# Kernel optimization log

Measured on AMD Instinct MI355X. Metric: run time of the kernel, lower is better.

## Reference

```python
import jax, jax.numpy as jnp
import numpy as np

THR = 0.01        # config['thr']
BORDER_RM = 2     # config['border_rm']
TEMP = 0.1        # config['dsmax_temperature']


def setup_inputs() -> dict:
    key = jax.random.key(0)
    k0, k1 = jax.random.split(key)
    N, C = 2, 256
    h0c, w0c, h1c, w1c = 60, 80, 60, 80
    feat_c0 = jax.random.normal(k0, (N, h0c * w0c, C), dtype=jnp.float32)
    feat_c1 = jax.random.normal(k1, (N, h1c * w1c, C), dtype=jnp.float32)
    return {"feat_c0": feat_c0, "feat_c1": feat_c1,
            "h0c": h0c, "w0c": w0c, "h1c": h1c, "w1c": w1c}


def _mask_border(m, b):
    # m: [N, H0, W0, H1, W1] bool; zero out a border of width b on all 4 grid axes
    m = m.at[:, :b].set(False)
    m = m.at[:, :, :b].set(False)
    m = m.at[:, :, :, :b].set(False)
    m = m.at[:, :, :, :, :b].set(False)
    m = m.at[:, -b:].set(False)
    m = m.at[:, :, -b:].set(False)
    m = m.at[:, :, :, -b:].set(False)
    m = m.at[:, :, :, :, -b:].set(False)
    return m


def reference(feat_c0, feat_c1, h0c, w0c, h1c, w1c):
    N, L, C = feat_c0.shape
    S = feat_c1.shape[1]
    # feats are each scaled by C**-0.5, then similarity divided by temperature
    sim = jnp.einsum('nlc,nsc->nls', feat_c0, feat_c1) / (C * TEMP)
    # dual softmax
    conf = jax.nn.softmax(sim, axis=1) * jax.nn.softmax(sim, axis=2)  # [N,L,S]

    # threshold + border removal
    mask = conf > THR
    mask = _mask_border(mask.reshape(N, h0c, w0c, h1c, w1c), BORDER_RM)
    mask = mask.reshape(N, L, S)

    # mutual nearest neighbour
    mask = mask & (conf == conf.max(axis=2, keepdims=True)) \
                & (conf == conf.max(axis=1, keepdims=True))

    # dense, fixed-shape match extraction (torch version uses torch.where)
    mask_v = mask.any(axis=2)                       # [N,L] bool: row i of batch b matched
    all_j = jnp.argmax(mask, axis=2)                # [N,L] matched column index
    mconf = jnp.where(
        mask_v,
        jnp.take_along_axis(conf, all_j[..., None], axis=2)[..., 0],
        jnp.zeros((), conf.dtype))                  # [N,L] match confidence (0 if unmatched)
    return conf, mask_v, all_j.astype(jnp.int32), mconf
```

## Files before the change

kernel.cpp:

```cpp
#include <hip/hip_runtime.h>
#include <hip/hip_bf16.h>
#include <stdint.h>

#define N_B   2
#define L_DIM 4800
#define S_DIM 4800
#define C_DIM 256
#define H0 60
#define W0 80
#define H1 60
#define W1 80
#define BORDER 2
#define THR 0.01f
#define SIM_SCALE 0.0390625f

typedef __attribute__((ext_vector_type(8))) short bf16x8;
typedef __attribute__((ext_vector_type(4))) float f32x4;

#define OFF_A  0
#define OFF_B  4915200
#define OFF_RS 9830400
#define OFF_CS 9868800
#define OFF_CM 9907200
#define OFF_RA 9945600
#define ZERO_BYTES 192000

__device__ __forceinline__ unsigned short f2bf_rne(float x) {
    unsigned int u = __float_as_uint(x);
    unsigned int r = (u + 0x7fffu + ((u >> 16) & 1u)) >> 16;
    return (unsigned short)r;
}

__global__ __launch_bounds__(256)
void convert_kernel(const float* __restrict__ f0, const float* __restrict__ f1,
                    unsigned short* __restrict__ a, unsigned short* __restrict__ b) {
    int idx = blockIdx.x * 256 + threadIdx.x;
    int i = idx * 4;
    float4 va = *reinterpret_cast<const float4*>(f0 + i);
    float4 vb = *reinterpret_cast<const float4*>(f1 + i);
    ushort4 ha, hb;
    ha.x = f2bf_rne(va.x); ha.y = f2bf_rne(va.y); ha.z = f2bf_rne(va.z); ha.w = f2bf_rne(va.w);
    hb.x = f2bf_rne(vb.x); hb.y = f2bf_rne(vb.y); hb.z = f2bf_rne(vb.z); hb.w = f2bf_rne(vb.w);
    *reinterpret_cast<ushort4*>(a + i) = ha;
    *reinterpret_cast<ushort4*>(b + i) = hb;
}

template <int PASS>
__global__ __launch_bounds__(256)
void gemm_pass(const unsigned short* __restrict__ A,
               const unsigned short* __restrict__ B,
               float* __restrict__ rowsum, float* __restrict__ colsum,
               unsigned long long* __restrict__ rowarg,
               unsigned int* __restrict__ colmaxbits,
               float* __restrict__ conf_out) {
    const int n      = blockIdx.z;
    const int tile_r = blockIdx.y * 96;
    const int tile_c = blockIdx.x * 96;
    const int lane   = threadIdx.x & 63;
    const int w      = threadIdx.x >> 6;
    const int wr     = w >> 1, wc = w & 1;
    const int base_r = tile_r + wr * 48;
    const int base_c = tile_c + wc * 48;
    const int lrow   = lane & 15;
    const int kgrp   = lane >> 4;

    const unsigned short* Abase = A + (size_t)n * L_DIM * C_DIM;
    const unsigned short* Bbase = B + (size_t)n * S_DIM * C_DIM;

    f32x4 acc[3][3] = {};

    #pragma unroll
    for (int kk = 0; kk < 8; ++kk) {
        const int k0 = kk * 32 + kgrp * 8;
        bf16x8 af[3], bf[3];
        #pragma unroll
        for (int f = 0; f < 3; ++f) {
            af[f] = *reinterpret_cast<const bf16x8*>(
                Abase + (size_t)(base_r + f * 16 + lrow) * C_DIM + k0);
            bf[f] = *reinterpret_cast<const bf16x8*>(
                Bbase + (size_t)(base_c + f * 16 + lrow) * C_DIM + k0);
        }
        #pragma unroll
        for (int i = 0; i < 3; ++i)
            #pragma unroll
            for (int j = 0; j < 3; ++j)
                acc[i][j] = __builtin_amdgcn_mfma_f32_16x16x32_bf16(af[i], bf[j], acc[i][j], 0, 0, 0);
    }

    if (PASS == 1) {
        float rsum[3][4];
        float csum[3];
        #pragma unroll
        for (int i = 0; i < 3; ++i)
            #pragma unroll
            for (int q = 0; q < 4; ++q) rsum[i][q] = 0.f;
        #pragma unroll
        for (int j = 0; j < 3; ++j) csum[j] = 0.f;

        #pragma unroll
        for (int i = 0; i < 3; ++i)
            #pragma unroll
            for (int j = 0; j < 3; ++j)
                #pragma unroll
                for (int q = 0; q < 4; ++q) {
                    float e = __expf(acc[i][j][q] * SIM_SCALE);
                    rsum[i][q] += e;
                    csum[j]    += e;
                }

        #pragma unroll
        for (int m = 1; m < 16; m <<= 1)
            #pragma unroll
            for (int i = 0; i < 3; ++i)
                #pragma unroll
                for (int q = 0; q < 4; ++q)
                    rsum[i][q] += __shfl_xor(rsum[i][q], m, 64);
        if (lrow == 0) {
            #pragma unroll
            for (int i = 0; i < 3; ++i)
                #pragma unroll
                for (int q = 0; q < 4; ++q)
                    atomicAdd(&rowsum[(size_t)n * L_DIM + base_r + i * 16 + kgrp * 4 + q],
                              rsum[i][q]);
        }
        #pragma unroll
        for (int m = 16; m < 64; m <<= 1)
            #pragma unroll
            for (int j = 0; j < 3; ++j)
                csum[j] += __shfl_xor(csum[j], m, 64);
        if (kgrp == 0) {
            #pragma unroll
            for (int j = 0; j < 3; ++j)
                atomicAdd(&colsum[(size_t)n * S_DIM + base_c + j * 16 + lrow], csum[j]);
        }
    } else {
        float irs[3][4];
        #pragma unroll
        for (int i = 0; i < 3; ++i)
            #pragma unroll
            for (int q = 0; q < 4; ++q)
                irs[i][q] = 1.0f / rowsum[(size_t)n * L_DIM + base_r + i * 16 + kgrp * 4 + q];
        float ics[3];
        #pragma unroll
        for (int j = 0; j < 3; ++j)
            ics[j] = 1.0f / colsum[(size_t)n * S_DIM + base_c + j * 16 + lrow];

        unsigned long long rmax[3][4];
        #pragma unroll
        for (int i = 0; i < 3; ++i)
            #pragma unroll
            for (int q = 0; q < 4; ++q) rmax[i][q] = 0ull;
        float cmax[3] = {0.f, 0.f, 0.f};

        #pragma unroll
        for (int i = 0; i < 3; ++i)
            #pragma unroll
            for (int j = 0; j < 3; ++j)
                #pragma unroll
                for (int q = 0; q < 4; ++q) {
                    float e    = __expf(acc[i][j][q] * SIM_SCALE);
                    float conf = (e * e) * irs[i][q] * ics[j];
                    int row = base_r + i * 16 + kgrp * 4 + q;
                    int col = base_c + j * 16 + lrow;
                    conf_out[((size_t)n * L_DIM + row) * S_DIM + col] = conf;
                    unsigned long long p =
                        ((unsigned long long)__float_as_uint(conf) << 32) | (unsigned)col;
                    if (p > rmax[i][q]) rmax[i][q] = p;
                    if (conf > cmax[j]) cmax[j] = conf;
                }

        #pragma unroll
        for (int m = 1; m < 16; m <<= 1)
            #pragma unroll
            for (int i = 0; i < 3; ++i)
                #pragma unroll
                for (int q = 0; q < 4; ++q) {
                    unsigned long long o = __shfl_xor(rmax[i][q], m, 64);
                    if (o > rmax[i][q]) rmax[i][q] = o;
                }
        if (lrow == 0) {
            #pragma unroll
            for (int i = 0; i < 3; ++i)
                #pragma unroll
                for (int q = 0; q < 4; ++q)
                    atomicMax(&rowarg[(size_t)n * L_DIM + base_r + i * 16 + kgrp * 4 + q],
                              rmax[i][q]);
        }
        #pragma unroll
        for (int m = 16; m < 64; m <<= 1)
            #pragma unroll
            for (int j = 0; j < 3; ++j) {
                float o = __shfl_xor(cmax[j], m, 64);
                if (o > cmax[j]) cmax[j] = o;
            }
        if (kgrp == 0) {
            #pragma unroll
            for (int j = 0; j < 3; ++j)
                atomicMax(&colmaxbits[(size_t)n * S_DIM + base_c + j * 16 + lrow],
                          __float_as_uint(cmax[j]));
        }
    }
}

__global__ __launch_bounds__(256)
void finalize_kernel(const unsigned long long* __restrict__ rowarg,
                     const unsigned int* __restrict__ colmaxbits,
                     float* __restrict__ out_maskv,
                     float* __restrict__ out_allj,
                     float* __restrict__ out_mconf) {
    int idx = blockIdx.x * 256 + threadIdx.x;
    if (idx >= N_B * L_DIM) return;
    int n = idx / L_DIM;
    int l = idx - n * L_DIM;
    unsigned long long p = rowarg[idx];
    unsigned int cbits = (unsigned int)(p >> 32);
    int s = (int)(p & 0xffffffffu);
    float cv = __uint_as_float(cbits);
    int i0 = l / W0, j0 = l - i0 * W0;
    int i1 = s / W1, j1 = s - i1 * W1;
    bool border = (i0 >= BORDER) && (i0 < H0 - BORDER) &&
                  (j0 >= BORDER) && (j0 < W0 - BORDER) &&
                  (i1 >= BORDER) && (i1 < H1 - BORDER) &&
                  (j1 >= BORDER) && (j1 < W1 - BORDER);
    bool matched = (cv > THR) && border && (colmaxbits[n * S_DIM + s] == cbits);
    out_maskv[idx] = matched ? 1.0f : 0.0f;
    out_allj[idx]  = matched ? (float)s : 0.0f;
    out_mconf[idx] = matched ? cv : 0.0f;
}

extern "C" void kernel_launch(void* const* d_in, const int* in_sizes, int n_in,
                              void* d_out, int out_size, void* d_ws, size_t ws_size,
                              hipStream_t stream) {
    const float* f0 = (const float*)d_in[0];
    const float* f1 = (const float*)d_in[1];
    float* out = (float*)d_out;

    char* ws = (char*)d_ws;
    unsigned short*     Abf        = (unsigned short*)(ws + OFF_A);
    unsigned short*     Bbf        = (unsigned short*)(ws + OFF_B);
    float*              rowsum     = (float*)(ws + OFF_RS);
    float*              colsum     = (float*)(ws + OFF_CS);
    unsigned int*       colmaxbits = (unsigned int*)(ws + OFF_CM);
    unsigned long long* rowarg     = (unsigned long long*)(ws + OFF_RA);

    hipMemsetAsync(ws + OFF_RS, 0, ZERO_BYTES, stream);

    convert_kernel<<<2400, 256, 0, stream>>>(f0, f1, Abf, Bbf);

    dim3 grid(S_DIM / 96, L_DIM / 96, N_B);
    gemm_pass<1><<<grid, 256, 0, stream>>>(Abf, Bbf, rowsum, colsum,
                                           nullptr, nullptr, nullptr);
    gemm_pass<2><<<grid, 256, 0, stream>>>(Abf, Bbf, rowsum, colsum,
                                           rowarg, colmaxbits, out);

    const size_t CONF_ELEMS = (size_t)N_B * L_DIM * S_DIM;
    float* out_maskv = out + CONF_ELEMS;
    float* out_allj  = out_maskv + (size_t)N_B * L_DIM;
    float* out_mconf = out_allj  + (size_t)N_B * L_DIM;
    finalize_kernel<<<(N_B * L_DIM + 255) / 256, 256, 0, stream>>>(
        rowarg, colmaxbits, out_maskv, out_allj, out_mconf);
}
```

Before: 458.5 us.

## Stage GEMM tiles through double-buffered LDS with larger 192x192 block tiles

The two GEMM passes now use 512-thread blocks with 192x192 output tiles. A and B K-slices are staged into shared memory through direct global-to-LDS loads, double-buffered across the K loop, and each wave reads its fragments from LDS instead of from global memory. This raises operand reuse and cuts redundant global and L2 traffic in the compute-heavy passes. In exchange, each wave keeps 18 accumulator fragments, which raises register pressure, and the grid shrinks to 25x25x2 blocks, which may underfill the GPU's compute units.

```diff
diff --git a/kernel.cpp b/kernel.cpp
--- a/kernel.cpp
+++ b/kernel.cpp
@@ -14,6 +14,13 @@
 #define THR 0.01f
 #define SIM_SCALE 0.0390625f
 
+#define TILE 192
+#define BK   32
+#define NK   8
+#define A_BYTES 12288
+#define PH_BYTES 24576
+#define CHUNKS_AB 1536
+
 typedef __attribute__((ext_vector_type(8))) short bf16x8;
 typedef __attribute__((ext_vector_type(4))) float f32x4;
 
@@ -29,6 +36,12 @@
     unsigned int u = __float_as_uint(x);
     unsigned int r = (u + 0x7fffu + ((u >> 16) & 1u)) >> 16;
     return (unsigned short)r;
+}
+
+__device__ __forceinline__ void gload16(const void* g, void* l) {
+    __builtin_amdgcn_global_load_lds(
+        (const __attribute__((address_space(1))) void*)g,
+        (__attribute__((address_space(3))) void*)l, 16, 0, 0);
 }
 
 __global__ __launch_bounds__(256)
@@ -46,122 +59,136 @@
 }
 
 template <int PASS>
-__global__ __launch_bounds__(256)
+__global__ __launch_bounds__(512)
 void gemm_pass(const unsigned short* __restrict__ A,
                const unsigned short* __restrict__ B,
                float* __restrict__ rowsum, float* __restrict__ colsum,
                unsigned long long* __restrict__ rowarg,
                unsigned int* __restrict__ colmaxbits,
                float* __restrict__ conf_out) {
+    __shared__ char smem[2 * PH_BYTES];
+
     const int n      = blockIdx.z;
-    const int tile_r = blockIdx.y * 96;
-    const int tile_c = blockIdx.x * 96;
-    const int lane   = threadIdx.x & 63;
-    const int w      = threadIdx.x >> 6;
-    const int wr     = w >> 1, wc = w & 1;
-    const int base_r = tile_r + wr * 48;
-    const int base_c = tile_c + wc * 48;
+    const int tile_r = blockIdx.y * TILE;
+    const int tile_c = blockIdx.x * TILE;
+    const int tid    = threadIdx.x;
+    const int lane   = tid & 63;
+    const int w      = tid >> 6;
+    const int wr     = w >> 2;
+    const int wc     = w & 3;
     const int lrow   = lane & 15;
     const int kgrp   = lane >> 4;
 
-    const unsigned short* Abase = A + (size_t)n * L_DIM * C_DIM;
-    const unsigned short* Bbase = B + (size_t)n * S_DIM * C_DIM;
-
-    f32x4 acc[3][3] = {};
-
+    const unsigned short* Abase = A + (size_t)n * L_DIM * C_DIM + (size_t)tile_r * C_DIM;
+    const unsigned short* Bbase = B + (size_t)n * S_DIM * C_DIM + (size_t)tile_c * C_DIM;
+
+    f32x4 acc[6][3] = {};
+
+#define STAGE(PH, KK)                                                          \
+    {                                                                          \
+        const int kbase = (KK) * BK;                                           \
+        _Pragma("unroll")                                                      \
+        for (int r = 0; r < 3; ++r) {                                          \
+            int idx = r * 512 + tid;                                           \
+            int ci  = (idx < 768) ? idx : idx - 768;                           \
+            int row = ci >> 2;                                                 \
+            int kc  = ci & 3;                                                  \
+            const unsigned short* src =                                        \
+                ((idx < 768) ? Abase : Bbase) + (size_t)row * C_DIM + kbase + kc * 8; \
+            gload16(src, smem + (PH) * PH_BYTES + idx * 16);                   \
+        }                                                                      \
+    }
+
+    STAGE(0, 0)
     #pragma unroll
-    for (int kk = 0; kk < 8; ++kk) {
-        const int k0 = kk * 32 + kgrp * 8;
-        bf16x8 af[3], bf[3];
-        #pragma unroll
-        for (int f = 0; f < 3; ++f) {
-            af[f] = *reinterpret_cast<const bf16x8*>(
-                Abase + (size_t)(base_r + f * 16 + lrow) * C_DIM + k0);
-            bf[f] = *reinterpret_cast<const bf16x8*>(
-                Bbase + (size_t)(base_c + f * 16 + lrow) * C_DIM + k0);
-        }
-        #pragma unroll
-        for (int i = 0; i < 3; ++i)
-            #pragma unroll
-            for (int j = 0; j < 3; ++j)
-                acc[i][j] = __builtin_amdgcn_mfma_f32_16x16x32_bf16(af[i], bf[j], acc[i][j], 0, 0, 0);
+    for (int kk = 0; kk < NK; ++kk) {
+        __syncthreads();
+        const int phase = kk & 1;
+        if (kk + 1 < NK) STAGE(phase ^ 1, kk + 1)
+
+        const char* pa = smem + phase * PH_BYTES;
+        bf16x8 af[6], bb[3];
+        #pragma unroll
+        for (int i = 0; i < 6; ++i)
+            af[i] = *reinterpret_cast<const bf16x8*>(
+                pa + ((wr * 96 + i * 16 + lrow) * 4 + kgrp) * 16);
+        #pragma unroll
+        for (int j = 0; j < 3; ++j)
+            bb[j] = *reinterpret_cast<const bf16x8*>(
+                pa + A_BYTES + ((wc * 48 + j * 16 + lrow) * 4 + kgrp) * 16);
+        #pragma unroll
+        for (int i = 0; i < 6; ++i)
+            #pragma unroll
+            for (int j = 0; j < 3; ++j)
+                acc[i][j] = __builtin_amdgcn_mfma_f32_16x16x32_bf16(
+                    af[i], bb[j], acc[i][j], 0, 0, 0);
     }
+#undef STAGE
 
     if (PASS == 1) {
-        float rsum[3][4];
-        float csum[3];
-        #pragma unroll
-        for (int i = 0; i < 3; ++i)
-            #pragma unroll
-            for (int q = 0; q < 4; ++q) rsum[i][q] = 0.f;
-        #pragma unroll
-        for (int j = 0; j < 3; ++j) csum[j] = 0.f;
-
-        #pragma unroll
-        for (int i = 0; i < 3; ++i)
+        float rs[6][4] = {};
+        float cs[3]    = {};
+        #pragma unroll
+        for (int i = 0; i < 6; ++i)
             #pragma unroll
             for (int j = 0; j < 3; ++j)
                 #pragma unroll
                 for (int q = 0; q < 4; ++q) {
                     float e = __expf(acc[i][j][q] * SIM_SCALE);
-                    rsum[i][q] += e;
-                    csum[j]    += e;
+                    rs[i][q] += e;
+                    cs[j]    += e;
                 }
-
         #pragma unroll
         for (int m = 1; m < 16; m <<= 1)
             #pragma unroll
-            for (int i = 0; i < 3; ++i)
+            for (int i = 0; i < 6; ++i)
                 #pragma unroll
                 for (int q = 0; q < 4; ++q)
-                    rsum[i][q] += __shfl_xor(rsum[i][q], m, 64);
+                    rs[i][q] += __shfl_xor(rs[i][q], m, 64);
         if (lrow == 0) {
             #pragma unroll
-            for (int i = 0; i < 3; ++i)
+            for (int i = 0; i < 6; ++i)
                 #pragma unroll
                 for (int q = 0; q < 4; ++q)
-                    atomicAdd(&rowsum[(size_t)n * L_DIM + base_r + i * 16 + kgrp * 4 + q],
-                              rsum[i][q]);
+                    atomicAdd(&rowsum[(size_t)n * L_DIM + tile_r + wr * 96 + i * 16 + kgrp * 4 + q],
+                              rs[i][q]);
         }
         #pragma unroll
         for (int m = 16; m < 64; m <<= 1)
             #pragma unroll
             for (int j = 0; j < 3; ++j)
-                csum[j] += __shfl_xor(csum[j], m, 64);
+                cs[j] += __shfl_xor(cs[j], m, 64);
         if (kgrp == 0) {
             #pragma unroll
             for (int j = 0; j < 3; ++j)
-                atomicAdd(&colsum[(size_t)n * S_DIM + base_c + j * 16 + lrow], csum[j]);
+                atomicAdd(&colsum[(size_t)n * S_DIM + tile_c + wc * 48 + j * 16 + lrow], cs[j]);
         }
     } else {
-        float irs[3][4];
-        #pragma unroll
-        for (int i = 0; i < 3; ++i)
+        float irs[6][4];
+        #pragma unroll
+        for (int i = 0; i < 6; ++i)
             #pragma unroll
             for (int q = 0; q < 4; ++q)
-                irs[i][q] = 1.0f / rowsum[(size_t)n * L_DIM + base_r + i * 16 + kgrp * 4 + q];
+                irs[i][q] = 1.0f /
+                    rowsum[(size_t)n * L_DIM + tile_r + wr * 96 + i * 16 + kgrp * 4 + q];
         float ics[3];
         #pragma unroll
         for (int j = 0; j < 3; ++j)
-            ics[j] = 1.0f / colsum[(size_t)n * S_DIM + base_c + j * 16 + lrow];
-
-        unsigned long long rmax[3][4];
-        #pragma unroll
-        for (int i = 0; i < 3; ++i)
-            #pragma unroll
-            for (int q = 0; q < 4; ++q) rmax[i][q] = 0ull;
-        float cmax[3] = {0.f, 0.f, 0.f};
-
-        #pragma unroll
-        for (int i = 0; i < 3; ++i)
+            ics[j] = 1.0f / colsum[(size_t)n * S_DIM + tile_c + wc * 48 + j * 16 + lrow];
+
+        unsigned long long rmax[6][4] = {};
+        float cmax[3] = {};
+
+        #pragma unroll
+        for (int i = 0; i < 6; ++i)
             #pragma unroll
             for (int j = 0; j < 3; ++j)
                 #pragma unroll
                 for (int q = 0; q < 4; ++q) {
                     float e    = __expf(acc[i][j][q] * SIM_SCALE);
                     float conf = (e * e) * irs[i][q] * ics[j];
-                    int row = base_r + i * 16 + kgrp * 4 + q;
-                    int col = base_c + j * 16 + lrow;
+                    int row = tile_r + wr * 96 + i * 16 + kgrp * 4 + q;
+                    int col = tile_c + wc * 48 + j * 16 + lrow;
                     conf_out[((size_t)n * L_DIM + row) * S_DIM + col] = conf;
                     unsigned long long p =
                         ((unsigned long long)__float_as_uint(conf) << 32) | (unsigned)col;
@@ -172,7 +199,7 @@
         #pragma unroll
         for (int m = 1; m < 16; m <<= 1)
             #pragma unroll
-            for (int i = 0; i < 3; ++i)
+            for (int i = 0; i < 6; ++i)
                 #pragma unroll
                 for (int q = 0; q < 4; ++q) {
                     unsigned long long o = __shfl_xor(rmax[i][q], m, 64);
@@ -180,10 +207,10 @@
                 }
         if (lrow == 0) {
             #pragma unroll
-            for (int i = 0; i < 3; ++i)
+            for (int i = 0; i < 6; ++i)
                 #pragma unroll
                 for (int q = 0; q < 4; ++q)
-                    atomicMax(&rowarg[(size_t)n * L_DIM + base_r + i * 16 + kgrp * 4 + q],
+                    atomicMax(&rowarg[(size_t)n * L_DIM + tile_r + wr * 96 + i * 16 + kgrp * 4 + q],
                               rmax[i][q]);
         }
         #pragma unroll
@@ -196,7 +223,7 @@
         if (kgrp == 0) {
             #pragma unroll
             for (int j = 0; j < 3; ++j)
-                atomicMax(&colmaxbits[(size_t)n * S_DIM + base_c + j * 16 + lrow],
+                atomicMax(&colmaxbits[(size_t)n * S_DIM + tile_c + wc * 48 + j * 16 + lrow],
                           __float_as_uint(cmax[j]));
         }
     }
@@ -247,10 +274,10 @@
 
     convert_kernel<<<2400, 256, 0, stream>>>(f0, f1, Abf, Bbf);
 
-    dim3 grid(S_DIM / 96, L_DIM / 96, N_B);
-    gemm_pass<1><<<grid, 256, 0, stream>>>(Abf, Bbf, rowsum, colsum,
+    dim3 grid(S_DIM / TILE, L_DIM / TILE, N_B);
+    gemm_pass<1><<<grid, 512, 0, stream>>>(Abf, Bbf, rowsum, colsum,
                                            nullptr, nullptr, nullptr);
-    gemm_pass<2><<<grid, 256, 0, stream>>>(Abf, Bbf, rowsum, colsum,
+    gemm_pass<2><<<grid, 512, 0, stream>>>(Abf, Bbf, rowsum, colsum,
                                            rowarg, colmaxbits, out);
 
     const size_t CONF_ELEMS = (size_t)N_B * L_DIM * S_DIM;
```

Result: faster. 386.3 us (-15.7%).
